# Performance work log

Hardware: AMD Instinct MI355X
Metric: run time of the kernel (lower is better)

The kernel has to match this reference:

```python
import jax, jax.numpy as jnp
import numpy as np

B, L, D_MODEL = 1, 1024, 768
H = 12            # num_heads == num_key_value_heads
FDIM = 16         # feature_dim
HEAD_DIM = D_MODEL // H  # 64
EPS = 1e-12
R2 = np.sqrt(2.0)
RD = np.sqrt(float(FDIM))        # sqrt(16) = 4
RRD = np.sqrt(RD)                # sqrt(4) = 2


def setup_inputs() -> dict:
    key = jax.random.key(0)
    ks = jax.random.split(key, 5)
    s = 1.0 / np.sqrt(D_MODEL)
    return {
        "hidden_states": jax.random.normal(ks[0], (B, L, D_MODEL), dtype=jnp.float32),
        "Wq": jax.random.normal(ks[1], (D_MODEL, H * FDIM), dtype=jnp.float32) * s,
        "Wk": jax.random.normal(ks[2], (D_MODEL, H * FDIM), dtype=jnp.float32) * s,
        "Wv": jax.random.normal(ks[3], (D_MODEL, D_MODEL), dtype=jnp.float32) * s,
        "Wo": jax.random.normal(ks[4], (D_MODEL, D_MODEL), dtype=jnp.float32) * s,
    }


def taylor_exp_feature_map(x):
    # x: (b, h, l, FDIM) -> (b, h, l, 1 + FDIM + FDIM^2)
    x2 = (x[..., :, None] * x[..., None, :]).reshape(*x.shape[:-1], FDIM * FDIM) / R2
    ones = jnp.ones((*x.shape[:-1], 1), dtype=x.dtype)
    return jnp.concatenate([ones, x / RRD, x2 / RD], axis=-1)


def reference(hidden_states, Wq, Wk, Wv, Wo):
    b, l, _ = hidden_states.shape
    q = (hidden_states @ Wq).reshape(b, l, H, FDIM).transpose(0, 2, 1, 3)
    k = (hidden_states @ Wk).reshape(b, l, H, FDIM).transpose(0, 2, 1, 3)
    v = (hidden_states @ Wv).reshape(b, l, H, HEAD_DIM).transpose(0, 2, 1, 3)
    q = taylor_exp_feature_map(q)  # (b,h,l,Dexp)
    k = taylor_exp_feature_map(k)  # (b,h,l,Dexp)
    # causal linear attention: y_t = q_t . cumsum_t(k_s v_s^T) / (q_t . cumsum_t(k_s) + eps)
    kv = k[..., :, None] * v[..., None, :]          # (b,h,l,Dexp,hd)
    kv_cum = jnp.cumsum(kv, axis=2)                  # (b,h,l,Dexp,hd)
    num = jnp.einsum('bhln,bhlnd->bhld', q, kv_cum)  # (b,h,l,hd)
    k_cum = jnp.cumsum(k, axis=2)                    # (b,h,l,Dexp)
    den = jnp.einsum('bhln,bhln->bhl', q, k_cum)[..., None] + EPS
    y = num / den                                    # (b,h,l,hd)
    y = y.transpose(0, 2, 1, 3).reshape(b, l, H * HEAD_DIM)
    return y @ Wo
```

## Files before the change

### kernel.cpp

```cpp
#include <hip/hip_runtime.h>

#define C2 0.17677669529663687f

typedef __attribute__((ext_vector_type(8))) short short8;
typedef __attribute__((ext_vector_type(8))) unsigned short ushort8;
typedef __attribute__((ext_vector_type(4))) float f32x4;

__device__ __forceinline__ unsigned short f2bf(float x) {
    union { float f; unsigned u; } v; v.f = x;
    unsigned r = v.u + 0x7fffu + ((v.u >> 16) & 1u);
    return (unsigned short)(r >> 16);
}
__device__ __forceinline__ float bf2f(unsigned short u) {
    union { unsigned u; float f; } v; v.u = ((unsigned)u) << 16;
    return v.f;
}

__global__ __launch_bounds__(512) void cvt_prep(
    const float* __restrict__ hs, const float* __restrict__ Wq, const float* __restrict__ Wk,
    const float* __restrict__ Wv, const float* __restrict__ Wo,
    unsigned short* __restrict__ Hh, unsigned short* __restrict__ Wqh,
    unsigned short* __restrict__ Wkh, unsigned short* __restrict__ Wvh,
    unsigned short* __restrict__ Woh)
{
    int e8 = (blockIdx.x * 512 + threadIdx.x) * 8;
    const float* src; unsigned short* dst; int off;
    if      (e8 < 786432)  { src = hs; dst = Hh;  off = e8; }
    else if (e8 < 933888)  { src = Wq; dst = Wqh; off = e8 - 786432; }
    else if (e8 < 1081344) { src = Wk; dst = Wkh; off = e8 - 933888; }
    else if (e8 < 1671168) { src = Wv; dst = Wvh; off = e8 - 1081344; }
    else                   { src = Wo; dst = Woh; off = e8 - 1671168; }
    float4 a = *(const float4*)&src[off];
    float4 b = *(const float4*)&src[off + 4];
    ushort8 o;
    o[0] = f2bf(a.x); o[1] = f2bf(a.y); o[2] = f2bf(a.z); o[3] = f2bf(a.w);
    o[4] = f2bf(b.x); o[5] = f2bf(b.y); o[6] = f2bf(b.z); o[7] = f2bf(b.w);
    *(ushort8*)&dst[off] = o;
}

__device__ __forceinline__ void gemm_inblk_splitk_h(
    const unsigned short* __restrict__ A,
    const unsigned short* __restrict__ W,
    float* __restrict__ out, unsigned short* __restrict__ outh,
    int row0, int n0, int outcol0, int ldw, int outld, bool write_f32)
{
    __shared__ __align__(16) unsigned short Al[2][2][3][64][40];
    __shared__ __align__(16) unsigned short Bl[2][2][3][64][40];
    float (*red)[65] = (float (*)[65])&Bl[0][0][0][0][0];
    const int tid = threadIdx.x;
    const int g = tid >> 8;
    const int t = tid & 255;
    const int lane = t & 63, wave4 = t >> 6;
    const int wm = wave4 & 1, wn = wave4 >> 1;
    const int quad = lane >> 4, lr = lane & 15;
    const int k0base = g * 384;
    const int ar = t >> 2, ak8 = (t & 3) * 8;
    const int bkr = t >> 3, bn8 = (t & 7) * 8;

    f32x4 acc[2][2] = {{{0.f,0.f,0.f,0.f},{0.f,0.f,0.f,0.f}},
                       {{0.f,0.f,0.f,0.f},{0.f,0.f,0.f,0.f}}};

    #pragma unroll
    for (int sk = 0; sk < 3; ++sk) {
        ushort8 ra = *(const ushort8*)&A[(size_t)(row0 + ar) * 768 + k0base + sk * 32 + ak8];
        ushort8 rb = *(const ushort8*)&W[(size_t)(k0base + sk * 32 + bkr) * ldw + n0 + bn8];
        *(ushort8*)&Al[g][0][sk][ar][ak8] = ra;
        #pragma unroll
        for (int j = 0; j < 8; ++j) {
            int n = bn8 + j;
            int col = (((bkr >> 3) ^ (n >> 4)) << 3) | (bkr & 7);
            Bl[g][0][sk][n][col] = rb[j];
        }
    }
    __syncthreads();

    const int ITER = 4;
    #pragma unroll
    for (int i = 0; i < ITER; ++i) {
        const int cur = i & 1, nxt = cur ^ 1;
        ushort8 na[3], nb[3];
        if (i + 1 < ITER) {
            int kn = k0base + (i + 1) * 96;
            #pragma unroll
            for (int sk = 0; sk < 3; ++sk) {
                na[sk] = *(const ushort8*)&A[(size_t)(row0 + ar) * 768 + kn + sk * 32 + ak8];
                nb[sk] = *(const ushort8*)&W[(size_t)(kn + sk * 32 + bkr) * ldw + n0 + bn8];
            }
        }
        #pragma unroll
        for (int sk = 0; sk < 3; ++sk) {
            short8 af[2], bfr[2];
            #pragma unroll
            for (int mi = 0; mi < 2; ++mi)
                af[mi] = *(const short8*)&Al[g][cur][sk][wm * 32 + mi * 16 + lr][quad << 3];
            #pragma unroll
            for (int ni = 0; ni < 2; ++ni) {
                int csw = quad ^ ((wn * 2 + ni) & 3);
                bfr[ni] = *(const short8*)&Bl[g][cur][sk][wn * 32 + ni * 16 + lr][csw << 3];
            }
            #pragma unroll
            for (int mi = 0; mi < 2; ++mi)
                #pragma unroll
                for (int ni = 0; ni < 2; ++ni)
                    acc[mi][ni] = __builtin_amdgcn_mfma_f32_16x16x32_bf16(af[mi], bfr[ni], acc[mi][ni], 0, 0, 0);
        }
        if (i + 1 < ITER) {
            #pragma unroll
            for (int sk = 0; sk < 3; ++sk) {
                *(ushort8*)&Al[g][nxt][sk][ar][ak8] = na[sk];
                #pragma unroll
                for (int j = 0; j < 8; ++j) {
                    int n = bn8 + j;
                    int col = (((bkr >> 3) ^ (n >> 4)) << 3) | (bkr & 7);
                    Bl[g][nxt][sk][n][col] = nb[sk][j];
                }
            }
        }
        __syncthreads();
    }
    if (g == 1) {
        #pragma unroll
        for (int mi = 0; mi < 2; ++mi)
            #pragma unroll
            for (int ni = 0; ni < 2; ++ni)
                #pragma unroll
                for (int r = 0; r < 4; ++r)
                    red[wm * 32 + mi * 16 + quad * 4 + r][wn * 32 + ni * 16 + lr] = acc[mi][ni][r];
    }
    __syncthreads();
    if (g == 0) {
        #pragma unroll
        for (int mi = 0; mi < 2; ++mi)
            #pragma unroll
            for (int ni = 0; ni < 2; ++ni)
                #pragma unroll
                for (int r = 0; r < 4; ++r) {
                    int rr = wm * 32 + mi * 16 + quad * 4 + r;
                    int cc = wn * 32 + ni * 16 + lr;
                    float v = acc[mi][ni][r] + red[rr][cc];
                    if (write_f32) out[(size_t)(row0 + rr) * outld + outcol0 + cc] = v;
                    if (outh) outh[(size_t)(row0 + rr) * outld + outcol0 + cc] = f2bf(v);
                }
    }
}

__global__ __launch_bounds__(512) void gemm_qkv_mfma(
    const unsigned short* __restrict__ Hh, const unsigned short* __restrict__ Wqh,
    const unsigned short* __restrict__ Wkh, const unsigned short* __restrict__ Wvh,
    float* __restrict__ out, unsigned short* __restrict__ outh)
{
    const int nt = blockIdx.x, mt = blockIdx.y;
    const unsigned short* W; int ldw, n0;
    if (nt < 3)      { W = Wqh; ldw = 192; n0 = nt * 64; }
    else if (nt < 6) { W = Wkh; ldw = 192; n0 = (nt - 3) * 64; }
    else             { W = Wvh; ldw = 768; n0 = (nt - 6) * 64; }
    gemm_inblk_splitk_h(Hh, W, out, outh, mt * 64, n0, nt * 64, ldw, 1152, nt < 6);
}

__global__ __launch_bounds__(512) void gemm_wo_mfma(
    const unsigned short* __restrict__ Yh, const unsigned short* __restrict__ Woh,
    float* __restrict__ out)
{
    const int nt = blockIdx.x, mt = blockIdx.y;
    gemm_inblk_splitk_h(Yh, Woh, out, (unsigned short*)nullptr,
                        mt * 64, nt * 64, nt * 64, 768, 768, true);
}

__global__ __launch_bounds__(512) void chunk_state_k(
    const float* __restrict__ qkv, const unsigned short* __restrict__ qkvh,
    unsigned short* __restrict__ St, float* __restrict__ zb)
{
    const int c = blockIdx.x, h = blockIdx.y;
    __shared__ float Kc[64][17];
    __shared__ unsigned short Pk[320][72];
    __shared__ unsigned short Vt[80][72];
    const int tid = threadIdx.x;
    const int lane = tid & 63, wave = tid >> 6;
    const int quad = lane >> 4, lr = lane & 15;

    if (tid < 256) {
        int s = tid >> 2, f4 = (tid & 3) * 4;
        float4 kv = *(const float4*)&qkv[(size_t)(c * 64 + s) * 1152 + 192 + h * 16 + f4];
        Kc[s][f4 + 0] = kv.x; Kc[s][f4 + 1] = kv.y; Kc[s][f4 + 2] = kv.z; Kc[s][f4 + 3] = kv.w;
    }
    {
        int s = tid >> 3, d8 = (tid & 7) * 8;
        ushort8 vv = *(const ushort8*)&qkvh[(size_t)(c * 64 + s) * 1152 + 384 + h * 64 + d8];
        #pragma unroll
        for (int j = 0; j < 8; ++j) Vt[d8 + j][s] = vv[j];
    }
    for (int idx = tid; idx < 16 * 72; idx += 512) {
        int rr = 64 + idx / 72, ss = idx % 72;
        Vt[rr][ss] = (rr == 64 && ss < 64) ? (unsigned short)0x3F80 : (unsigned short)0;
    }
    __syncthreads();
    for (int idx = tid; idx < 2880; idx += 512) {
        int n = idx / 9, s8 = (idx % 9) * 8;
        short8 v8;
        #pragma unroll
        for (int tt = 0; tt < 8; ++tt) {
            int s = s8 + tt;
            float ph = 0.f;
            if (s < 64 && n < 273) {
                if (n == 0) ph = 1.f;
                else if (n < 17) ph = Kc[s][n - 1] * 0.5f;
                else { int m = n - 17; ph = Kc[s][m >> 4] * Kc[s][m & 15] * C2; }
            }
            v8[tt] = (short)f2bf(ph);
        }
        *(short8*)&Pk[n][s8] = v8;
    }
    __syncthreads();

    f32x4 acc[5][3];
    #pragma unroll
    for (int mt = 0; mt < 5; ++mt)
        #pragma unroll
        for (int nt = 0; nt < 3; ++nt) acc[mt][nt] = (f32x4){0.f, 0.f, 0.f, 0.f};
    #pragma unroll
    for (int ks = 0; ks < 2; ++ks) {
        short8 af[5], bfr[3];
        #pragma unroll
        for (int mt = 0; mt < 5; ++mt)
            af[mt] = *(const short8*)&Vt[mt * 16 + lr][ks * 32 + quad * 8];
        #pragma unroll
        for (int nt = 0; nt < 3; ++nt)
            if (wave + 8 * nt < 20)
                bfr[nt] = *(const short8*)&Pk[(wave + 8 * nt) * 16 + lr][ks * 32 + quad * 8];
        #pragma unroll
        for (int mt = 0; mt < 5; ++mt)
            #pragma unroll
            for (int nt = 0; nt < 3; ++nt)
                if (wave + 8 * nt < 20)
                    acc[mt][nt] = __builtin_amdgcn_mfma_f32_16x16x32_bf16(af[mt], bfr[nt], acc[mt][nt], 0, 0, 0);
    }
    unsigned short* Sbt = St + (size_t)(h * 16 + c) * 18432;
    float* zp = zb + (h * 16 + c) * 273;
    #pragma unroll
    for (int nt = 0; nt < 3; ++nt) {
        int tile = wave + 8 * nt;
        if (tile < 20) {
            int n = tile * 16 + lr;
            if (n < 288) {
                #pragma unroll
                for (int mt = 0; mt < 4; ++mt)
                    #pragma unroll
                    for (int r = 0; r < 4; ++r)
                        Sbt[(mt * 16 + quad * 4 + r) * 288 + n] =
                            (n < 273) ? f2bf(acc[mt][nt][r]) : (unsigned short)0;
                if (quad == 0 && n < 273) zp[n] = acc[4][nt][0];
            }
        }
    }
}

__global__ __launch_bounds__(256) void scan_state_k(unsigned short* __restrict__ St, float* __restrict__ z)
{
    const int NV = 12 * 64 * 36;
    int gid = blockIdx.x * 256 + threadIdx.x;
    if (gid < NV) {
        int hh = gid / (64 * 36), rem = gid % (64 * 36);
        int d = rem / 36, nb = rem % 36;
        unsigned short* p = St + (size_t)hh * 16 * 18432 + d * 288 + nb * 8;
        ushort8 v[16];
        #pragma unroll
        for (int cc = 0; cc < 16; ++cc) v[cc] = *(const ushort8*)(p + (size_t)cc * 18432);
        float run[8] = {0.f,0.f,0.f,0.f,0.f,0.f,0.f,0.f};
        #pragma unroll
        for (int cc = 0; cc < 16; ++cc) {
            ushort8 w;
            #pragma unroll
            for (int j = 0; j < 8; ++j) {
                w[j] = f2bf(run[j]);
                run[j] += bf2f(v[cc][j]);
            }
            *(ushort8*)(p + (size_t)cc * 18432) = w;
        }
    } else if (gid < NV + 12 * 273) {
        int e2 = gid - NV, hh = e2 / 273, n = e2 % 273;
        float* p = z + hh * 16 * 273 + n;
        float v[16];
        #pragma unroll
        for (int cc = 0; cc < 16; ++cc) v[cc] = p[cc * 273];
        float run = 0.f;
        #pragma unroll
        for (int cc = 0; cc < 16; ++cc) { p[cc * 273] = run; run += v[cc]; }
    }
}

__global__ __launch_bounds__(512) void chunk_out_k(
    const float* __restrict__ qkv, const unsigned short* __restrict__ qkvh,
    const unsigned short* __restrict__ St, const float* __restrict__ z,
    unsigned short* __restrict__ y)
{
    const int c = blockIdx.x, h = blockIdx.y;
    __shared__ float Qc[64][17];
    __shared__ unsigned short Aq[64][40];
    __shared__ unsigned short Kb[64][40];
    __shared__ unsigned short Pq[64][360];
    __shared__ unsigned short Vt[64][72];
    __shared__ float zl[288];
    __shared__ float dpart[12][64];
    const int tid = threadIdx.x;
    const int lane = tid & 63, wave = tid >> 6;
    const int quad = lane >> 4, lr = lane & 15;
    const int wm = wave & 1, wn = wave >> 1;

    const unsigned short* Sgt = St + (size_t)(h * 16 + c) * 18432;
    short8 sfr[9];
    #pragma unroll
    for (int ks = 0; ks < 9; ++ks)
        sfr[ks] = *(const short8*)&Sgt[(wn * 16 + lr) * 288 + ks * 32 + quad * 8];

    if (tid < 256) {
        int s = tid >> 2, f4 = (tid & 3) * 4;
        float4 qv = *(const float4*)&qkv[(size_t)(c * 64 + s) * 1152 + h * 16 + f4];
        Qc[s][f4 + 0] = qv.x; Qc[s][f4 + 1] = qv.y; Qc[s][f4 + 2] = qv.z; Qc[s][f4 + 3] = qv.w;
        *(ushort4*)&Aq[s][f4] =
            *(const ushort4*)&qkvh[(size_t)(c * 64 + s) * 1152 + h * 16 + f4];
        *(ushort4*)&Kb[s][f4] =
            *(const ushort4*)&qkvh[(size_t)(c * 64 + s) * 1152 + 192 + h * 16 + f4];
        *(ushort4*)&Aq[s][16 + (tid & 3) * 4] = make_ushort4(0, 0, 0, 0);
        *(ushort4*)&Kb[s][16 + (tid & 3) * 4] = make_ushort4(0, 0, 0, 0);
    }
    {
        int ss = tid >> 3, d8 = (tid & 7) * 8;
        ushort8 vv = *(const ushort8*)&qkvh[(size_t)(c * 64 + ss) * 1152 + 384 + h * 64 + d8];
        #pragma unroll
        for (int j = 0; j < 8; ++j) Vt[d8 + j][ss] = vv[j];
    }
    const float* zg = z + (h * 16 + c) * 273;
    for (int idx = tid; idx < 288; idx += 512) zl[idx] = (idx < 273) ? zg[idx] : 0.f;
    __syncthreads();

    f32x4 accS[2] = {{0.f,0.f,0.f,0.f},{0.f,0.f,0.f,0.f}};
    {
        short8 bfr = *(const short8*)&Kb[wn * 16 + lr][quad * 8];
        #pragma unroll
        for (int mi = 0; mi < 2; ++mi) {
            short8 af = *(const short8*)&Aq[wm * 32 + mi * 16 + lr][quad * 8];
            accS[mi] = __builtin_amdgcn_mfma_f32_16x16x32_bf16(af, bfr, accS[mi], 0, 0, 0);
        }
    }

    {
        int i = lane;
        float qr[16];
        #pragma unroll
        for (int f = 0; f < 16; ++f) qr[f] = Qc[i][f];
        float dp = 0.f;
        int n0 = wave * 36;
        for (int n = n0; n < n0 + 36; ++n) {
            float ph;
            if (n == 0) ph = 1.f;
            else if (n < 17) ph = qr[n - 1] * 0.5f;
            else if (n < 273) { int m = n - 17; ph = qr[m >> 4] * qr[m & 15] * C2; }
            else ph = 0.f;
            Pq[i][n] = f2bf(ph);
            dp += ph * zl[n];
        }
        dpart[wave][i] = dp;
    }

    #pragma unroll
    for (int mi = 0; mi < 2; ++mi) {
        float rs[4];
        #pragma unroll
        for (int r = 0; r < 4; ++r) {
            int i = wm * 32 + mi * 16 + quad * 4 + r;
            int j = wn * 16 + lr;
            float u = accS[mi][r];
            float sc = (j <= i) ? (1.f + 0.25f * u + u * u * (1.f / 32.f)) : 0.f;
            rs[r] = sc;
            Pq[i][288 + j] = f2bf(sc);
        }
        #pragma unroll
        for (int r = 0; r < 4; ++r) {
            float v = rs[r];
            v += __shfl_xor(v, 1);
            v += __shfl_xor(v, 2);
            v += __shfl_xor(v, 4);
            v += __shfl_xor(v, 8);
            if (lr == 0) dpart[8 + wn][wm * 32 + mi * 16 + quad * 4 + r] = v;
        }
    }
    __syncthreads();

    f32x4 acc[2] = {{0.f,0.f,0.f,0.f},{0.f,0.f,0.f,0.f}};
    __builtin_amdgcn_s_setprio(1);
    #pragma unroll
    for (int ks = 0; ks < 11; ++ks) {
        short8 bfr = (ks < 9)
            ? sfr[ks]
            : *(const short8*)&Vt[wn * 16 + lr][(ks - 9) * 32 + quad * 8];
        #pragma unroll
        for (int mi = 0; mi < 2; ++mi) {
            short8 af = *(const short8*)&Pq[wm * 32 + mi * 16 + lr][ks * 32 + quad * 8];
            acc[mi] = __builtin_amdgcn_mfma_f32_16x16x32_bf16(af, bfr, acc[mi], 0, 0, 0);
        }
    }
    __builtin_amdgcn_s_setprio(0);

    #pragma unroll
    for (int mi = 0; mi < 2; ++mi)
        #pragma unroll
        for (int r = 0; r < 4; ++r) {
            int i = wm * 32 + mi * 16 + quad * 4 + r;
            float den = 1e-12f;
            #pragma unroll
            for (int w = 0; w < 12; ++w) den += dpart[w][i];
            float rden = 1.f / den;
            y[(size_t)(c * 64 + i) * 768 + h * 64 + wn * 16 + lr] = f2bf(acc[mi][r] * rden);
        }
}

extern "C" void kernel_launch(void* const* d_in, const int* in_sizes, int n_in,
                              void* d_out, int out_size, void* d_ws, size_t ws_size,
                              hipStream_t stream) {
    const float* hs = (const float*)d_in[0];
    const float* Wq = (const float*)d_in[1];
    const float* Wk = (const float*)d_in[2];
    const float* Wv = (const float*)d_in[3];
    const float* Wo = (const float*)d_in[4];
    float* out = (float*)d_out;
    float* ws  = (float*)d_ws;

    float*          qkv  = ws;
    unsigned short* qkvh = (unsigned short*)(ws + 1179648);
    unsigned short* yb   = (unsigned short*)(ws + 1769472);
    unsigned short* St   = (unsigned short*)(ws + 2162688);
    float*          zb   = ws + 3932160;
    unsigned short* Hh   = (unsigned short*)(ws + 3984576);
    unsigned short* Wqh  = (unsigned short*)(ws + 4377792);
    unsigned short* Wkh  = (unsigned short*)(ws + 4451520);
    unsigned short* Wvh  = (unsigned short*)(ws + 4525248);
    unsigned short* Woh  = (unsigned short*)(ws + 4820160);

    cvt_prep     <<<552, 512, 0, stream>>>(hs, Wq, Wk, Wv, Wo, Hh, Wqh, Wkh, Wvh, Woh);
    gemm_qkv_mfma<<<dim3(18, 16), 512, 0, stream>>>(Hh, Wqh, Wkh, Wvh, qkv, qkvh);
    chunk_state_k<<<dim3(16, 12), 512, 0, stream>>>(qkv, qkvh, St, zb);
    scan_state_k <<<121, 256, 0, stream>>>(St, zb);
    chunk_out_k  <<<dim3(16, 12), 512, 0, stream>>>(qkv, qkvh, St, zb, yb);
    gemm_wo_mfma <<<dim3(12, 16), 512, 0, stream>>>(yb, Woh, out);
}
```

Measured before the change: 119.4 us.

## Fold inter-chunk prefix scan into chunk_out and drop scan kernel

Removes the separate scan_state_k launch. chunk_out_k now sums the per-chunk states of all earlier chunks itself and stages the result in shared memory, so each block does its own exclusive prefix. chunk_state_k writes its state tile through shared memory for coalesced ushort8 global stores. This saves one launch and one global read-write pass, but later chunks read up to 15 prior states, which unbalances work and adds redundant global traffic and extra LDS use.

```diff
diff --git a/kernel.cpp b/kernel.cpp
--- a/kernel.cpp
+++ b/kernel.cpp
@@ -174,6 +174,7 @@
     __shared__ float Kc[64][17];
     __shared__ unsigned short Pk[320][72];
     __shared__ unsigned short Vt[80][72];
+    unsigned short (*Sal)[288] = (unsigned short (*)[288])&Pk[0][0];
     const int tid = threadIdx.x;
     const int lane = tid & 63, wave = tid >> 6;
     const int quad = lane >> 4, lr = lane & 15;
@@ -234,7 +235,8 @@
                 if (wave + 8 * nt < 20)
                     acc[mt][nt] = __builtin_amdgcn_mfma_f32_16x16x32_bf16(af[mt], bfr[nt], acc[mt][nt], 0, 0, 0);
     }
-    unsigned short* Sbt = St + (size_t)(h * 16 + c) * 18432;
+    __syncthreads();
+
     float* zp = zb + (h * 16 + c) * 273;
     #pragma unroll
     for (int nt = 0; nt < 3; ++nt) {
@@ -246,51 +248,28 @@
                 for (int mt = 0; mt < 4; ++mt)
                     #pragma unroll
                     for (int r = 0; r < 4; ++r)
-                        Sbt[(mt * 16 + quad * 4 + r) * 288 + n] =
+                        Sal[mt * 16 + quad * 4 + r][n] =
                             (n < 273) ? f2bf(acc[mt][nt][r]) : (unsigned short)0;
                 if (quad == 0 && n < 273) zp[n] = acc[4][nt][0];
             }
         }
     }
-}
-
-__global__ __launch_bounds__(256) void scan_state_k(unsigned short* __restrict__ St, float* __restrict__ z)
-{
-    const int NV = 12 * 64 * 36;
-    int gid = blockIdx.x * 256 + threadIdx.x;
-    if (gid < NV) {
-        int hh = gid / (64 * 36), rem = gid % (64 * 36);
-        int d = rem / 36, nb = rem % 36;
-        unsigned short* p = St + (size_t)hh * 16 * 18432 + d * 288 + nb * 8;
-        ushort8 v[16];
-        #pragma unroll
-        for (int cc = 0; cc < 16; ++cc) v[cc] = *(const ushort8*)(p + (size_t)cc * 18432);
-        float run[8] = {0.f,0.f,0.f,0.f,0.f,0.f,0.f,0.f};
-        #pragma unroll
-        for (int cc = 0; cc < 16; ++cc) {
-            ushort8 w;
-            #pragma unroll
-            for (int j = 0; j < 8; ++j) {
-                w[j] = f2bf(run[j]);
-                run[j] += bf2f(v[cc][j]);
-            }
-            *(ushort8*)(p + (size_t)cc * 18432) = w;
-        }
-    } else if (gid < NV + 12 * 273) {
-        int e2 = gid - NV, hh = e2 / 273, n = e2 % 273;
-        float* p = z + hh * 16 * 273 + n;
-        float v[16];
-        #pragma unroll
-        for (int cc = 0; cc < 16; ++cc) v[cc] = p[cc * 273];
-        float run = 0.f;
-        #pragma unroll
-        for (int cc = 0; cc < 16; ++cc) { p[cc * 273] = run; run += v[cc]; }
+    __syncthreads();
+
+    unsigned short* Sbt = St + (size_t)(h * 16 + c) * 18432;
+    #pragma unroll
+    for (int k = 0; k < 5; ++k) {
+        int u = k * 512 + tid;
+        if (u < 2304) {
+            int row = u / 36, col8 = (u % 36) * 8;
+            *(ushort8*)&Sbt[row * 288 + col8] = *(const ushort8*)&Sal[row][col8];
+        }
     }
 }
 
 __global__ __launch_bounds__(512) void chunk_out_k(
     const float* __restrict__ qkv, const unsigned short* __restrict__ qkvh,
-    const unsigned short* __restrict__ St, const float* __restrict__ z,
+    const unsigned short* __restrict__ St, const float* __restrict__ zb,
     unsigned short* __restrict__ y)
 {
     const int c = blockIdx.x, h = blockIdx.y;
@@ -298,6 +277,7 @@
     __shared__ unsigned short Aq[64][40];
     __shared__ unsigned short Kb[64][40];
     __shared__ unsigned short Pq[64][360];
+    __shared__ unsigned short Sl[64][296];
     __shared__ unsigned short Vt[64][72];
     __shared__ float zl[288];
     __shared__ float dpart[12][64];
@@ -305,12 +285,6 @@
     const int lane = tid & 63, wave = tid >> 6;
     const int quad = lane >> 4, lr = lane & 15;
     const int wm = wave & 1, wn = wave >> 1;
-
-    const unsigned short* Sgt = St + (size_t)(h * 16 + c) * 18432;
-    short8 sfr[9];
-    #pragma unroll
-    for (int ks = 0; ks < 9; ++ks)
-        sfr[ks] = *(const short8*)&Sgt[(wn * 16 + lr) * 288 + ks * 32 + quad * 8];
 
     if (tid < 256) {
         int s = tid >> 2, f4 = (tid & 3) * 4;
@@ -329,8 +303,49 @@
         #pragma unroll
         for (int j = 0; j < 8; ++j) Vt[d8 + j][ss] = vv[j];
     }
-    const float* zg = z + (h * 16 + c) * 273;
-    for (int idx = tid; idx < 288; idx += 512) zl[idx] = (idx < 273) ? zg[idx] : 0.f;
+
+    {
+        const unsigned short* Sh = St + (size_t)h * 16 * 18432;
+        float sums[5][8];
+        #pragma unroll
+        for (int k = 0; k < 5; ++k)
+            #pragma unroll
+            for (int j = 0; j < 8; ++j) sums[k][j] = 0.f;
+        for (int cc = 0; cc < c; ++cc) {
+            const unsigned short* Sc = Sh + (size_t)cc * 18432;
+            ushort8 v[5];
+            #pragma unroll
+            for (int k = 0; k < 5; ++k) {
+                int u = k * 512 + tid;
+                if (u < 2304) {
+                    int row = u / 36, col8 = (u % 36) * 8;
+                    v[k] = *(const ushort8*)&Sc[row * 288 + col8];
+                }
+            }
+            #pragma unroll
+            for (int k = 0; k < 5; ++k)
+                if (k * 512 + tid < 2304)
+                    #pragma unroll
+                    for (int j = 0; j < 8; ++j) sums[k][j] += bf2f(v[k][j]);
+        }
+        #pragma unroll
+        for (int k = 0; k < 5; ++k) {
+            int u = k * 512 + tid;
+            if (u < 2304) {
+                int row = u / 36, col8 = (u % 36) * 8;
+                ushort8 w;
+                #pragma unroll
+                for (int j = 0; j < 8; ++j) w[j] = f2bf(sums[k][j]);
+                *(ushort8*)&Sl[row][col8] = w;
+            }
+        }
+    }
+    if (tid < 288) {
+        float run = 0.f;
+        if (tid < 273)
+            for (int cc = 0; cc < c; ++cc) run += zb[(h * 16 + cc) * 273 + tid];
+        zl[tid] = (tid < 273) ? run : 0.f;
+    }
     __syncthreads();
 
     f32x4 accS[2] = {{0.f,0.f,0.f,0.f},{0.f,0.f,0.f,0.f}};
@@ -391,7 +406,7 @@
     #pragma unroll
     for (int ks = 0; ks < 11; ++ks) {
         short8 bfr = (ks < 9)
-            ? sfr[ks]
+            ? *(const short8*)&Sl[wn * 16 + lr][ks * 32 + quad * 8]
             : *(const short8*)&Vt[wn * 16 + lr][(ks - 9) * 32 + quad * 8];
         #pragma unroll
         for (int mi = 0; mi < 2; ++mi) {
@@ -439,7 +454,6 @@
     cvt_prep     <<<552, 512, 0, stream>>>(hs, Wq, Wk, Wv, Wo, Hh, Wqh, Wkh, Wvh, Woh);
     gemm_qkv_mfma<<<dim3(18, 16), 512, 0, stream>>>(Hh, Wqh, Wkh, Wvh, qkv, qkvh);
     chunk_state_k<<<dim3(16, 12), 512, 0, stream>>>(qkv, qkvh, St, zb);
-    scan_state_k <<<121, 256, 0, stream>>>(St, zb);
     chunk_out_k  <<<dim3(16, 12), 512, 0, stream>>>(qkv, qkvh, St, zb, yb);
     gemm_wo_mfma <<<dim3(12, 16), 512, 0, stream>>>(yb, Woh, out);
 }
```

After: 130.5 us. +9.3%, slower.

## Fuse fp32-to-bf16 conversion into QKV GEMM loads and drop prep kernel

Applied to the files above, without the earlier changes.

Removes the separate conversion kernel. The QKV GEMM now reads fp32 hidden states and weights directly and converts them to bf16 while staging into shared memory. The Wo conversion is folded into extra blocks of the chunk_state kernel, so it overlaps with attention work. This saves a launch and a full bf16 round trip through global memory. In exchange, the GEMM reads twice the bytes per tile, and each of the 16 row-tile blocks converts the same weight tiles again.

```diff
diff --git a/kernel.cpp b/kernel.cpp
--- a/kernel.cpp
+++ b/kernel.cpp
@@ -16,31 +16,9 @@
     return v.f;
 }
 
-__global__ __launch_bounds__(512) void cvt_prep(
-    const float* __restrict__ hs, const float* __restrict__ Wq, const float* __restrict__ Wk,
-    const float* __restrict__ Wv, const float* __restrict__ Wo,
-    unsigned short* __restrict__ Hh, unsigned short* __restrict__ Wqh,
-    unsigned short* __restrict__ Wkh, unsigned short* __restrict__ Wvh,
-    unsigned short* __restrict__ Woh)
-{
-    int e8 = (blockIdx.x * 512 + threadIdx.x) * 8;
-    const float* src; unsigned short* dst; int off;
-    if      (e8 < 786432)  { src = hs; dst = Hh;  off = e8; }
-    else if (e8 < 933888)  { src = Wq; dst = Wqh; off = e8 - 786432; }
-    else if (e8 < 1081344) { src = Wk; dst = Wkh; off = e8 - 933888; }
-    else if (e8 < 1671168) { src = Wv; dst = Wvh; off = e8 - 1081344; }
-    else                   { src = Wo; dst = Woh; off = e8 - 1671168; }
-    float4 a = *(const float4*)&src[off];
-    float4 b = *(const float4*)&src[off + 4];
-    ushort8 o;
-    o[0] = f2bf(a.x); o[1] = f2bf(a.y); o[2] = f2bf(a.z); o[3] = f2bf(a.w);
-    o[4] = f2bf(b.x); o[5] = f2bf(b.y); o[6] = f2bf(b.z); o[7] = f2bf(b.w);
-    *(ushort8*)&dst[off] = o;
-}
-
-__device__ __forceinline__ void gemm_inblk_splitk_h(
-    const unsigned short* __restrict__ A,
-    const unsigned short* __restrict__ W,
+__device__ __forceinline__ void gemm_inblk_splitk_f(
+    const float* __restrict__ A,
+    const float* __restrict__ W,
     float* __restrict__ out, unsigned short* __restrict__ outh,
     int row0, int n0, int outcol0, int ldw, int outld, bool write_f32)
 {
@@ -62,14 +40,21 @@
 
     #pragma unroll
     for (int sk = 0; sk < 3; ++sk) {
-        ushort8 ra = *(const ushort8*)&A[(size_t)(row0 + ar) * 768 + k0base + sk * 32 + ak8];
-        ushort8 rb = *(const ushort8*)&W[(size_t)(k0base + sk * 32 + bkr) * ldw + n0 + bn8];
-        *(ushort8*)&Al[g][0][sk][ar][ak8] = ra;
+        const float* pa = &A[(size_t)(row0 + ar) * 768 + k0base + sk * 32 + ak8];
+        float4 a0 = *(const float4*)pa, a1 = *(const float4*)(pa + 4);
+        const float* pb = &W[(size_t)(k0base + sk * 32 + bkr) * ldw + n0 + bn8];
+        float4 b0 = *(const float4*)pb, b1 = *(const float4*)(pb + 4);
+        ushort8 ua;
+        ua[0] = f2bf(a0.x); ua[1] = f2bf(a0.y); ua[2] = f2bf(a0.z); ua[3] = f2bf(a0.w);
+        ua[4] = f2bf(a1.x); ua[5] = f2bf(a1.y); ua[6] = f2bf(a1.z); ua[7] = f2bf(a1.w);
+        *(ushort8*)&Al[g][0][sk][ar][ak8] = ua;
+        unsigned short ub[8] = { f2bf(b0.x), f2bf(b0.y), f2bf(b0.z), f2bf(b0.w),
+                                 f2bf(b1.x), f2bf(b1.y), f2bf(b1.z), f2bf(b1.w) };
         #pragma unroll
         for (int j = 0; j < 8; ++j) {
             int n = bn8 + j;
             int col = (((bkr >> 3) ^ (n >> 4)) << 3) | (bkr & 7);
-            Bl[g][0][sk][n][col] = rb[j];
+            Bl[g][0][sk][n][col] = ub[j];
         }
     }
     __syncthreads();
@@ -78,13 +63,15 @@
     #pragma unroll
     for (int i = 0; i < ITER; ++i) {
         const int cur = i & 1, nxt = cur ^ 1;
-        ushort8 na[3], nb[3];
+        float4 na[3][2], nb[3][2];
         if (i + 1 < ITER) {
             int kn = k0base + (i + 1) * 96;
             #pragma unroll
             for (int sk = 0; sk < 3; ++sk) {
-                na[sk] = *(const ushort8*)&A[(size_t)(row0 + ar) * 768 + kn + sk * 32 + ak8];
-                nb[sk] = *(const ushort8*)&W[(size_t)(kn + sk * 32 + bkr) * ldw + n0 + bn8];
+                const float* pa = &A[(size_t)(row0 + ar) * 768 + kn + sk * 32 + ak8];
+                na[sk][0] = *(const float4*)pa; na[sk][1] = *(const float4*)(pa + 4);
+                const float* pb = &W[(size_t)(kn + sk * 32 + bkr) * ldw + n0 + bn8];
+                nb[sk][0] = *(const float4*)pb; nb[sk][1] = *(const float4*)(pb + 4);
             }
         }
         #pragma unroll
@@ -107,12 +94,21 @@
         if (i + 1 < ITER) {
             #pragma unroll
             for (int sk = 0; sk < 3; ++sk) {
-                *(ushort8*)&Al[g][nxt][sk][ar][ak8] = na[sk];
+                ushort8 ua;
+                ua[0] = f2bf(na[sk][0].x); ua[1] = f2bf(na[sk][0].y);
+                ua[2] = f2bf(na[sk][0].z); ua[3] = f2bf(na[sk][0].w);
+                ua[4] = f2bf(na[sk][1].x); ua[5] = f2bf(na[sk][1].y);
+                ua[6] = f2bf(na[sk][1].z); ua[7] = f2bf(na[sk][1].w);
+                *(ushort8*)&Al[g][nxt][sk][ar][ak8] = ua;
+                unsigned short ub[8] = { f2bf(nb[sk][0].x), f2bf(nb[sk][0].y),
+                                         f2bf(nb[sk][0].z), f2bf(nb[sk][0].w),
+                                         f2bf(nb[sk][1].x), f2bf(nb[sk][1].y),
+                                         f2bf(nb[sk][1].z), f2bf(nb[sk][1].w) };
                 #pragma unroll
                 for (int j = 0; j < 8; ++j) {
                     int n = bn8 + j;
                     int col = (((bkr >> 3) ^ (n >> 4)) << 3) | (bkr & 7);
-                    Bl[g][nxt][sk][n][col] = nb[sk][j];
+                    Bl[g][nxt][sk][n][col] = ub[j];
                 }
             }
         }
@@ -144,17 +140,121 @@
     }
 }
 
+__device__ __forceinline__ void gemm_inblk_splitk_h(
+    const unsigned short* __restrict__ A,
+    const unsigned short* __restrict__ W,
+    float* __restrict__ out,
+    int row0, int n0, int outcol0, int ldw, int outld)
+{
+    __shared__ __align__(16) unsigned short Al[2][2][3][64][40];
+    __shared__ __align__(16) unsigned short Bl[2][2][3][64][40];
+    float (*red)[65] = (float (*)[65])&Bl[0][0][0][0][0];
+    const int tid = threadIdx.x;
+    const int g = tid >> 8;
+    const int t = tid & 255;
+    const int lane = t & 63, wave4 = t >> 6;
+    const int wm = wave4 & 1, wn = wave4 >> 1;
+    const int quad = lane >> 4, lr = lane & 15;
+    const int k0base = g * 384;
+    const int ar = t >> 2, ak8 = (t & 3) * 8;
+    const int bkr = t >> 3, bn8 = (t & 7) * 8;
+
+    f32x4 acc[2][2] = {{{0.f,0.f,0.f,0.f},{0.f,0.f,0.f,0.f}},
+                       {{0.f,0.f,0.f,0.f},{0.f,0.f,0.f,0.f}}};
+
+    #pragma unroll
+    for (int sk = 0; sk < 3; ++sk) {
+        ushort8 ra = *(const ushort8*)&A[(size_t)(row0 + ar) * 768 + k0base + sk * 32 + ak8];
+        ushort8 rb = *(const ushort8*)&W[(size_t)(k0base + sk * 32 + bkr) * ldw + n0 + bn8];
+        *(ushort8*)&Al[g][0][sk][ar][ak8] = ra;
+        #pragma unroll
+        for (int j = 0; j < 8; ++j) {
+            int n = bn8 + j;
+            int col = (((bkr >> 3) ^ (n >> 4)) << 3) | (bkr & 7);
+            Bl[g][0][sk][n][col] = rb[j];
+        }
+    }
+    __syncthreads();
+
+    const int ITER = 4;
+    #pragma unroll
+    for (int i = 0; i < ITER; ++i) {
+        const int cur = i & 1, nxt = cur ^ 1;
+        ushort8 na[3], nb[3];
+        if (i + 1 < ITER) {
+            int kn = k0base + (i + 1) * 96;
+            #pragma unroll
+            for (int sk = 0; sk < 3; ++sk) {
+                na[sk] = *(const ushort8*)&A[(size_t)(row0 + ar) * 768 + kn + sk * 32 + ak8];
+                nb[sk] = *(const ushort8*)&W[(size_t)(kn + sk * 32 + bkr) * ldw + n0 + bn8];
+            }
+        }
+        #pragma unroll
+        for (int sk = 0; sk < 3; ++sk) {
+            short8 af[2], bfr[2];
+            #pragma unroll
+            for (int mi = 0; mi < 2; ++mi)
+                af[mi] = *(const short8*)&Al[g][cur][sk][wm * 32 + mi * 16 + lr][quad << 3];
+            #pragma unroll
+            for (int ni = 0; ni < 2; ++ni) {
+                int csw = quad ^ ((wn * 2 + ni) & 3);
+                bfr[ni] = *(const short8*)&Bl[g][cur][sk][wn * 32 + ni * 16 + lr][csw << 3];
+            }
+            #pragma unroll
+            for (int mi = 0; mi < 2; ++mi)
+                #pragma unroll
+                for (int ni = 0; ni < 2; ++ni)
+                    acc[mi][ni] = __builtin_amdgcn_mfma_f32_16x16x32_bf16(af[mi], bfr[ni], acc[mi][ni], 0, 0, 0);
+        }
+        if (i + 1 < ITER) {
+            #pragma unroll
+            for (int sk = 0; sk < 3; ++sk) {
+                *(ushort8*)&Al[g][nxt][sk][ar][ak8] = na[sk];
+                #pragma unroll
+                for (int j = 0; j < 8; ++j) {
+                    int n = bn8 + j;
+                    int col = (((bkr >> 3) ^ (n >> 4)) << 3) | (bkr & 7);
+                    Bl[g][nxt][sk][n][col] = nb[sk][j];
+                }
+            }
+        }
+        __syncthreads();
+    }
+    if (g == 1) {
+        #pragma unroll
+        for (int mi = 0; mi < 2; ++mi)
+            #pragma unroll
+            for (int ni = 0; ni < 2; ++ni)
+                #pragma unroll
+                for (int r = 0; r < 4; ++r)
+                    red[wm * 32 + mi * 16 + quad * 4 + r][wn * 32 + ni * 16 + lr] = acc[mi][ni][r];
+    }
+    __syncthreads();
+    if (g == 0) {
+        #pragma unroll
+        for (int mi = 0; mi < 2; ++mi)
+            #pragma unroll
+            for (int ni = 0; ni < 2; ++ni)
+                #pragma unroll
+                for (int r = 0; r < 4; ++r) {
+                    int rr = wm * 32 + mi * 16 + quad * 4 + r;
+                    int cc = wn * 32 + ni * 16 + lr;
+                    out[(size_t)(row0 + rr) * outld + outcol0 + cc] = acc[mi][ni][r] + red[rr][cc];
+                }
+    }
+}
+
 __global__ __launch_bounds__(512) void gemm_qkv_mfma(
-    const unsigned short* __restrict__ Hh, const unsigned short* __restrict__ Wqh,
-    const unsigned short* __restrict__ Wkh, const unsigned short* __restrict__ Wvh,
+    const float* __restrict__ H, const float* __restrict__ Wq,
+    const float* __restrict__ Wk, const float* __restrict__ Wv,
     float* __restrict__ out, unsigned short* __restrict__ outh)
 {
     const int nt = blockIdx.x, mt = blockIdx.y;
-    const unsigned short* W; int ldw, n0;
-    if (nt < 3)      { W = Wqh; ldw = 192; n0 = nt * 64; }
-    else if (nt < 6) { W = Wkh; ldw = 192; n0 = (nt - 3) * 64; }
-    else             { W = Wvh; ldw = 768; n0 = (nt - 6) * 64; }
-    gemm_inblk_splitk_h(Hh, W, out, outh, mt * 64, n0, nt * 64, ldw, 1152, nt < 6);
+    const float* W; int ldw, n0;
+    if (nt < 3)      { W = Wq; ldw = 192; n0 = nt * 64; }
+    else if (nt < 6) { W = Wk; ldw = 192; n0 = (nt - 3) * 64; }
+    else             { W = Wv; ldw = 768; n0 = (nt - 6) * 64; }
+    gemm_inblk_splitk_f(H, W, out, outh, mt * 64, n0, nt * 64, ldw, 1152, nt < 6);
 }
 
 __global__ __launch_bounds__(512) void gemm_wo_mfma(
@@ -162,14 +262,24 @@
     float* __restrict__ out)
 {
     const int nt = blockIdx.x, mt = blockIdx.y;
-    gemm_inblk_splitk_h(Yh, Woh, out, (unsigned short*)nullptr,
-                        mt * 64, nt * 64, nt * 64, 768, 768, true);
+    gemm_inblk_splitk_h(Yh, Woh, out, mt * 64, nt * 64, nt * 64, 768, 768);
 }
 
 __global__ __launch_bounds__(512) void chunk_state_k(
     const float* __restrict__ qkv, const unsigned short* __restrict__ qkvh,
+    const float* __restrict__ Wo, unsigned short* __restrict__ Woh,
     unsigned short* __restrict__ St, float* __restrict__ zb)
 {
+    if (blockIdx.y >= 12) {
+        int off = ((blockIdx.y - 12) * 16 + blockIdx.x) * 4096 + threadIdx.x * 8;
+        float4 a = *(const float4*)&Wo[off];
+        float4 b = *(const float4*)&Wo[off + 4];
+        ushort8 o;
+        o[0] = f2bf(a.x); o[1] = f2bf(a.y); o[2] = f2bf(a.z); o[3] = f2bf(a.w);
+        o[4] = f2bf(b.x); o[5] = f2bf(b.y); o[6] = f2bf(b.z); o[7] = f2bf(b.w);
+        *(ushort8*)&Woh[off] = o;
+        return;
+    }
     const int c = blockIdx.x, h = blockIdx.y;
     __shared__ float Kc[64][17];
     __shared__ unsigned short Pk[320][72];
@@ -430,15 +540,10 @@
     unsigned short* yb   = (unsigned short*)(ws + 1769472);
     unsigned short* St   = (unsigned short*)(ws + 2162688);
     float*          zb   = ws + 3932160;
-    unsigned short* Hh   = (unsigned short*)(ws + 3984576);
-    unsigned short* Wqh  = (unsigned short*)(ws + 4377792);
-    unsigned short* Wkh  = (unsigned short*)(ws + 4451520);
-    unsigned short* Wvh  = (unsigned short*)(ws + 4525248);
-    unsigned short* Woh  = (unsigned short*)(ws + 4820160);
-
-    cvt_prep     <<<552, 512, 0, stream>>>(hs, Wq, Wk, Wv, Wo, Hh, Wqh, Wkh, Wvh, Woh);
-    gemm_qkv_mfma<<<dim3(18, 16), 512, 0, stream>>>(Hh, Wqh, Wkh, Wvh, qkv, qkvh);
-    chunk_state_k<<<dim3(16, 12), 512, 0, stream>>>(qkv, qkvh, St, zb);
+    unsigned short* Woh  = (unsigned short*)(ws + 3984576);
+
+    gemm_qkv_mfma<<<dim3(18, 16), 512, 0, stream>>>(hs, Wq, Wk, Wv, qkv, qkvh);
+    chunk_state_k<<<dim3(16, 21), 512, 0, stream>>>(qkv, qkvh, Wo, Woh, St, zb);
     scan_state_k <<<121, 256, 0, stream>>>(St, zb);
     chunk_out_k  <<<dim3(16, 12), 512, 0, stream>>>(qkv, qkvh, St, zb, yb);
     gemm_wo_mfma <<<dim3(12, 16), 512, 0, stream>>>(yb, Woh, out);
```

New measurement: 121.0 us. No clear change (+1.3%).
